# Kernel optimization log

Measured on AMD Instinct MI355X. Metric: run time of the kernel, lower is better.

The kernel has to match this reference:

```python
import jax, jax.numpy as jnp
import numpy as np

N_QUBITS = 16
DIM = 1 << N_QUBITS
NUM_CLASSES = 23
BATCH = 64

# PauliZ sign table: wire 0 is the most-significant bit of the flattened index.
_idx = np.arange(DIM)
SIGNS = np.stack([1 - 2 * ((_idx >> (N_QUBITS - 1 - w)) & 1) for w in range(N_QUBITS)], axis=1).astype(np.float32)  # (DIM, 16)


def _rx_mat(theta):
    c = jnp.cos(theta / 2).astype(jnp.complex64)
    s = (-1j * jnp.sin(theta / 2)).astype(jnp.complex64)
    return jnp.stack([jnp.stack([c, s]), jnp.stack([s, c])])  # (2,2)


def _rot_mat(phi, theta, omega):
    ct = jnp.cos(theta / 2)
    st = jnp.sin(theta / 2)
    a = jnp.exp(-0.5j * (phi + omega)) * ct
    b = -jnp.exp(0.5j * (phi - omega)) * st
    c = jnp.exp(-0.5j * (phi - omega)) * st
    d = jnp.exp(0.5j * (phi + omega)) * ct
    return jnp.stack([jnp.stack([a, b]), jnp.stack([c, d])]).astype(jnp.complex64)


def _apply_1q(state, U, w):
    # state: (B, 2,...,2); shared 2x2 gate on wire w (axis w+1)
    st = jnp.tensordot(state, U, axes=[[w + 1], [1]])  # contracted axis moves to last
    return jnp.moveaxis(st, -1, w + 1)


def _apply_rx_batched(state, theta_b, w):
    # per-sample RX angles theta_b: (B,)
    half = theta_b / 2
    c = jnp.cos(half).astype(jnp.complex64)
    s = (-1j * jnp.sin(half)).astype(jnp.complex64)
    U = jnp.stack([jnp.stack([c, s], -1), jnp.stack([s, c], -1)], -2)  # (B,2,2)
    st = jnp.moveaxis(state, w + 1, -1)
    st = jnp.einsum('bji,b...i->b...j', U, st)
    return jnp.moveaxis(st, -1, w + 1)


def _apply_crx(state, theta, ctrl, tgt):
    s0 = jax.lax.index_in_dim(state, 0, axis=ctrl + 1, keepdims=False)
    s1 = jax.lax.index_in_dim(state, 1, axis=ctrl + 1, keepdims=False)
    tax = tgt + 1 if tgt < ctrl else tgt  # target axis after control axis removal
    U = _rx_mat(theta)
    s1 = jnp.moveaxis(jnp.tensordot(s1, U, axes=[[tax], [1]]), -1, tax)
    return jnp.stack([s0, s1], axis=ctrl + 1)


def _circuit(x, w0, x0, w1, x1):
    B = x.shape[0]
    state = jnp.zeros((B,) + (2,) * N_QUBITS, jnp.complex64)
    state = state.at[(slice(None),) + (0,) * N_QUBITS].set(1.0)
    for w, xc in ((w0, x0), (w1, x1)):
        for q in range(N_QUBITS):
            state = _apply_rx_batched(state, x[:, q], q)
        for q in range(N_QUBITS):
            state = _apply_1q(state, _rot_mat(w[q, 0], w[q, 1], w[q, 2]), q)
        for q in range(N_QUBITS):
            state = _apply_crx(state, xc[q], q, (q + 1) % N_QUBITS)
    probs = (state.real ** 2 + state.imag ** 2).reshape(B, DIM)
    return probs @ jnp.asarray(SIGNS)  # (B, 16) PauliZ expvals


def setup_inputs() -> dict:
    key = jax.random.key(0)
    ks = jax.random.split(key, 7)
    return {
        'x': jax.random.normal(ks[0], (BATCH, N_QUBITS), jnp.float32),
        'w0': jax.random.normal(ks[1], (N_QUBITS, 3), jnp.float32),
        'x0': jax.random.normal(ks[2], (N_QUBITS,), jnp.float32),
        'w1': jax.random.normal(ks[3], (N_QUBITS, 3), jnp.float32),
        'x1': jax.random.normal(ks[4], (N_QUBITS,), jnp.float32),
        'fc_w': jax.random.normal(ks[5], (NUM_CLASSES, N_QUBITS), jnp.float32) * 0.25,
        'fc_b': jax.random.normal(ks[6], (NUM_CLASSES,), jnp.float32) * 0.05,
    }


def reference(x, w0, x0, w1, x1, fc_w, fc_b):
    feats = _circuit(x, w0, x0, w1, x1)           # (B, 16)
    logits = feats @ fc_w.T + fc_b                # (B, 23)
    return jax.nn.log_softmax(logits, axis=1)
```

## Files before the change

kernel.cpp:

```cpp
#include <hip/hip_runtime.h>
#include <hip/hip_bf16.h>


#define DIM 65536
#define BATCH 64
#define PSTR 580


template<int RB>
__device__ __forceinline__ void g1q_reg(float* sr, float* si, const float* U) {
  float u00r=U[0],u00i=U[1],u01r=U[2],u01i=U[3],u10r=U[4],u10i=U[5],u11r=U[6],u11i=U[7];
#pragma unroll
  for (int k = 0; k < 8; ++k) {
    int lo = k & ((1<<RB)-1);
    int j0 = ((k >> RB) << (RB+1)) | lo;
    int j1 = j0 | (1<<RB);
    float a0r=sr[j0], a0i=si[j0], a1r=sr[j1], a1i=si[j1];
    sr[j0] = u00r*a0r - u00i*a0i + u01r*a1r - u01i*a1i;
    si[j0] = u00r*a0i + u00i*a0r + u01r*a1i + u01i*a1r;
    sr[j1] = u10r*a0r - u10i*a0i + u11r*a1r - u11i*a1i;
    si[j1] = u10r*a0i + u10i*a0r + u11r*a1i + u11i*a1r;
  }
}

template<int RB, int CB>
__device__ __forceinline__ void gsel_reg_cc(float* sr, float* si, const float* M0, const float* M1) {
  float a0=M0[0],a1=M0[1],a2=M0[2],a3=M0[3],a4=M0[4],a5=M0[5],a6=M0[6],a7=M0[7];
  float b0=M1[0],b1=M1[1],b2=M1[2],b3=M1[3],b4=M1[4],b5=M1[5],b6=M1[6],b7=M1[7];
#pragma unroll
  for (int k = 0; k < 8; ++k) {
    int lo = k & ((1<<RB)-1);
    int j0 = ((k >> RB) << (RB+1)) | lo;
    int j1 = j0 | (1<<RB);
    const bool c = ((j0 >> CB) & 1) != 0;
    float u00r=c?b0:a0, u00i=c?b1:a1, u01r=c?b2:a2, u01i=c?b3:a3;
    float u10r=c?b4:a4, u10i=c?b5:a5, u11r=c?b6:a6, u11i=c?b7:a7;
    float p0r=sr[j0], p0i=si[j0], p1r=sr[j1], p1i=si[j1];
    sr[j0] = u00r*p0r - u00i*p0i + u01r*p1r - u01i*p1i;
    si[j0] = u00r*p0i + u00i*p0r + u01r*p1i + u01i*p1r;
    sr[j1] = u10r*p0r - u10i*p0i + u11r*p1r - u11i*p1i;
    si[j1] = u10r*p0i + u10i*p0r + u11r*p1i + u11i*p1r;
  }
}

template<int RB>
__device__ __forceinline__ void gsel_reg_pred(float* sr, float* si, const float* M0,
                                              const float* M1, bool ctrl) {
  float u[8];
#pragma unroll
  for (int e = 0; e < 8; ++e) u[e] = ctrl ? M1[e] : M0[e];
  g1q_reg<RB>(sr, si, u);
}

template<int CB, int LB>
__device__ __forceinline__ void crx_reg_lane(float* sr, float* si, float c, float s) {
#pragma unroll
  for (int k = 0; k < 8; ++k) {
    int lo2 = k & ((1<<CB)-1);
    int j = ((((k >> CB) << (CB+1)) | lo2)) | (1<<CB);
    float pr = __shfl_xor(sr[j], 1<<LB, 64);
    float pi = __shfl_xor(si[j], 1<<LB, 64);
    float mr = sr[j], mi = si[j];
    sr[j] = c*mr + s*pi;
    si[j] = c*mi - s*pr;
  }
}

__device__ __forceinline__ int swz(int o) { return o ^ ((o>>4)&15) ^ ((o>>8)&15); }

__device__ __forceinline__ unsigned bfp(float r, float i) {
  unsigned ur = __float_as_uint(r), ui = __float_as_uint(i);
  ur = (ur + 0x7fffu + ((ur >> 16) & 1u)) >> 16;
  ui = (ui + 0x7fffu + ((ui >> 16) & 1u)) & 0xffff0000u;
  return (ur & 0xffffu) | ui;
}
__device__ __forceinline__ float bfr(unsigned u) { return __uint_as_float(u << 16); }
__device__ __forceinline__ float bfi(unsigned u) { return __uint_as_float(u & 0xffff0000u); }

#define MP(Pb, l, q, s) ((Pb) + (((l)*16+(q))*2+(s))*8)


__global__ __launch_bounds__(256) void pA(float2* __restrict__ pre2, float* __restrict__ P,
                                          const float* __restrict__ x, const float* __restrict__ w0,
                                          const float* __restrict__ x0, const float* __restrict__ w1,
                                          const float* __restrict__ x1, float* __restrict__ feats,
                                          int* __restrict__ ctr) {
  __shared__ float2 lds2[4096];
  int b = blockIdx.x;
  int t = threadIdx.x, lane = t & 63, wv = t >> 6;
  float* Pb = P + (size_t)b * PSTR;

  {
    float (*su)[8] = reinterpret_cast<float(*)[8]>(lds2);
    if (t < 16) feats[b*16 + t] = 0.f;
    if (t == 16) ctr[b] = 0;
    if (t < 32) {
      int l = t >> 4, q = t & 15;
      const float* W = (l ? w1 : w0) + q*3;
      float xa = 0.5f * x[b*16 + q];
      float cr = cosf(xa), sx = sinf(xa);
      float phi = W[0], th = W[1], om = W[2];
      float ct = cosf(0.5f*th), stt = sinf(0.5f*th);
      float po = 0.5f*(phi+om), pm = 0.5f*(phi-om);
      float ar =  cosf(po)*ct,  ai = -sinf(po)*ct;
      float br = -cosf(pm)*stt, bi = -sinf(pm)*stt;
      float cr2 = cosf(pm)*stt, ci2 = -sinf(pm)*stt;
      float dr =  cosf(po)*ct,  di =  sinf(po)*ct;
      float U[8];
      U[0] = ar*cr + bi*sx;   U[1] = ai*cr - br*sx;
      U[2] = ai*sx + br*cr;   U[3] = -ar*sx + bi*cr;
      U[4] = cr2*cr + di*sx;  U[5] = ci2*cr - dr*sx;
      U[6] = ci2*sx + dr*cr;  U[7] = -cr2*sx + di*cr;
      float* M0 = MP(Pb, l, q, 0);
      float* M1 = M0 + 8;
#pragma unroll
      for (int e = 0; e < 8; ++e) { M0[e] = U[e]; su[t][e] = U[e]; }
      if (q == 0) {
        float ang = l ? 0.5f*x0[15] : 0.f;
        float cg = cosf(ang), sg = sinf(ang);
        M1[0] =  cg*U[0] + sg*U[3];  M1[1] = cg*U[1] - sg*U[2];
        M1[2] =  sg*U[1] + cg*U[2];  M1[3] = -sg*U[0] + cg*U[3];
        M1[4] =  cg*U[4] + sg*U[7];  M1[5] = cg*U[5] - sg*U[6];
        M1[6] =  sg*U[5] + cg*U[6];  M1[7] = -sg*U[4] + cg*U[7];
      } else {
        float ang = 0.5f*(l ? x1[q-1] : x0[q-1]);
        float cg = cosf(ang), sg = sinf(ang);
        M1[0] = cg*U[0] + sg*U[5];  M1[1] = cg*U[1] - sg*U[4];
        M1[2] = cg*U[2] + sg*U[7];  M1[3] = cg*U[3] - sg*U[6];
        M1[4] = cg*U[4] + sg*U[1];  M1[5] = cg*U[5] - sg*U[0];
        M1[6] = cg*U[6] + sg*U[3];  M1[7] = cg*U[7] - sg*U[2];
      }
      if (t == 0) { Pb[576] = cosf(0.5f*x1[15]); Pb[577] = sinf(0.5f*x1[15]); }
    }
    __syncthreads();
    if (t == 0) {
      float T0r[8], T0i[8], T1r[8], T1i[8];
#pragma unroll
      for (int k = 0; k < 8; ++k) {
        int b2 = (k>>2)&1, b1 = (k>>1)&1, b0k = k&1;
        float xr = su[13][b2*4], xi = su[13][b2*4+1];
        float yr = su[14][b1*4], yi = su[14][b1*4+1];
        float zr = su[15][b0k*4], zi = su[15][b0k*4+1];
        float pr = xr*yr - xi*yi, pi = xr*yi + xi*yr;
        T0r[k] = pr*zr - pi*zi; T0i[k] = pr*zi + pi*zr;
      }
      float a12 = 0.5f*x0[12], c12 = cosf(a12), s12 = sinf(a12);
#pragma unroll
      for (int k = 0; k < 8; ++k) { T1r[k] = c12*T0r[k] + s12*T0i[k^4]; T1i[k] = c12*T0i[k] - s12*T0r[k^4]; }
      float a13 = 0.5f*x0[13], c13 = cosf(a13), s13 = sinf(a13);
      float n0r[8], n0i[8], n1r[8], n1i[8];
#pragma unroll
      for (int k = 0; k < 8; ++k) {
        if (k & 4) {
          n0r[k] = c13*T0r[k] + s13*T0i[k^2]; n0i[k] = c13*T0i[k] - s13*T0r[k^2];
          n1r[k] = c13*T1r[k] + s13*T1i[k^2]; n1i[k] = c13*T1i[k] - s13*T1r[k^2];
        } else { n0r[k]=T0r[k]; n0i[k]=T0i[k]; n1r[k]=T1r[k]; n1i[k]=T1i[k]; }
      }
      float a14 = 0.5f*x0[14], c14 = cosf(a14), s14 = sinf(a14);
      float Fr[2][8], Fi[2][8];
#pragma unroll
      for (int k = 0; k < 8; ++k) {
        float r0, i0, r1, i1;
        if (k & 2) {
          r0 = c14*n0r[k] + s14*n0i[k^1]; i0 = c14*n0i[k] - s14*n0r[k^1];
          r1 = c14*n1r[k] + s14*n1i[k^1]; i1 = c14*n1i[k] - s14*n1r[k^1];
        } else { r0=n0r[k]; i0=n0i[k]; r1=n1r[k]; i1=n1i[k]; }
        Fr[0][k] = r0; Fi[0][k] = i0; Fr[1][k] = r1; Fi[1][k] = i1;
      }
      const float* A = MP(Pb,0,12,0);
      const float* B = MP(Pb,0,12,1);
      float wr[2][2], wi[2][2];
      wr[0][0] = A[0]; wi[0][0] = A[1];  wr[1][0] = A[4]; wi[1][0] = A[5];
      wr[0][1] = B[0]; wi[0][1] = B[1];  wr[1][1] = B[4]; wi[1][1] = B[5];
      float* T2 = Pb + 512;
#pragma unroll
      for (int j0 = 0; j0 < 2; ++j0)
#pragma unroll
        for (int j1 = 0; j1 < 2; ++j1)
#pragma unroll
          for (int k = 0; k < 8; ++k) {
            float tr = Fr[j0][k], ti = Fi[j0][k];
            float fr = wr[j0][j1], fi = wi[j0][j1];
            T2[((j0*2 + j1)*8 + k)*2 + 0] = tr*fr - ti*fi;
            T2[((j0*2 + j1)*8 + k)*2 + 1] = tr*fi + ti*fr;
          }
    }
  }

  float sr[16], si[16];
#pragma unroll
  for (int r = 0; r < 16; ++r) { sr[r] = 0.f; si[r] = 0.f; }
  if (t == 0) sr[0] = 1.f;

  g1q_reg<3>(sr, si, MP(Pb,0,0,0));
  gsel_reg_cc<2,3>(sr, si, MP(Pb,0,1,0), MP(Pb,0,1,1));
  gsel_reg_cc<1,2>(sr, si, MP(Pb,0,2,0), MP(Pb,0,2,1));
  gsel_reg_cc<0,1>(sr, si, MP(Pb,0,3,0), MP(Pb,0,3,1));
  __syncthreads();
#pragma unroll
  for (int r = 0; r < 16; ++r) {
    int o = wv | (lane << 2) | (r << 8);
    lds2[swz(o) & 4095] = make_float2(sr[r], si[r]);
  }
  __syncthreads();
#pragma unroll
  for (int r = 0; r < 16; ++r) {
    int o = wv | (((lane>>4)&3) << 2) | (r << 4) | ((lane&15) << 8);
    float2 v = lds2[swz(o) & 4095]; sr[r] = v.x; si[r] = v.y;
  }
  gsel_reg_pred<3>(sr, si, MP(Pb,0,4,0), MP(Pb,0,4,1), (lane&1)!=0);
  gsel_reg_cc<2,3>(sr, si, MP(Pb,0,5,0), MP(Pb,0,5,1));
  gsel_reg_cc<1,2>(sr, si, MP(Pb,0,6,0), MP(Pb,0,6,1));
  gsel_reg_cc<0,1>(sr, si, MP(Pb,0,7,0), MP(Pb,0,7,1));
  __syncthreads();
#pragma unroll
  for (int r = 0; r < 16; ++r) {
    int o = wv | (((lane>>4)&3) << 2) | (r << 4) | ((lane&15) << 8);
    lds2[swz(o) & 4095] = make_float2(sr[r], si[r]);
  }
  __syncthreads();
#pragma unroll
  for (int r = 0; r < 16; ++r) {
    int o = r | (lane << 4) | (wv << 10);
    float2 v = lds2[swz(o) & 4095]; sr[r] = v.x; si[r] = v.y;
  }
  gsel_reg_pred<3>(sr, si, MP(Pb,0,8,0), MP(Pb,0,8,1), (lane&1)!=0);
  gsel_reg_cc<2,3>(sr, si, MP(Pb,0,9,0), MP(Pb,0,9,1));
  gsel_reg_cc<1,2>(sr, si, MP(Pb,0,10,0), MP(Pb,0,10,1));
  gsel_reg_cc<0,1>(sr, si, MP(Pb,0,11,0), MP(Pb,0,11,1));
#pragma unroll
  for (int r = 0; r < 16; ++r) {
    int paddr = ((lane>>4)&3) | (wv << 2) | (r << 4) | ((lane&15) << 8);
    pre2[(size_t)b*4096 + paddr] = make_float2(sr[r], si[r]);
  }
}


__global__ __launch_bounds__(512) void pB(unsigned* __restrict__ st, const float2* __restrict__ pre2,
                                          const float* __restrict__ P) {
  __shared__ float2 lds2[8192];
  int blk = blockIdx.x;
  int b = blk >> 3, m = blk & 7;
  int t = threadIdx.x, lane = t & 63, wv = t >> 6;
  const float* Pb = P + (size_t)b*PSTR;

  float sr[16], si[16];
  {
    const float4* src = (const float4*)(pre2 + (size_t)b*4096) + ((lane << 3) | ((wv&3) << 9));
#pragma unroll
    for (int g = 0; g < 8; ++g) {
      float4 v = src[g];
      sr[2*g] = v.x; si[2*g] = v.y; sr[2*g+1] = v.z; si[2*g+1] = v.w;
    }
    int k = ((wv>>2)&1) | ((m&3) << 1);
    const float* tf = Pb + 512 + ((((m>>2)&1)*2 + (lane&1))*8 + k)*2;
    float fr = tf[0], fi = tf[1];
    const float* M = ((wv>>2)&1) ? MP(Pb,1,0,1) : MP(Pb,1,0,0);
    float v8[8];
#pragma unroll
    for (int e = 0; e < 4; ++e) {
      v8[2*e]   = fr*M[2*e]   - fi*M[2*e+1];
      v8[2*e+1] = fr*M[2*e+1] + fi*M[2*e];
    }
    g1q_reg<3>(sr, si, v8);
  }
  gsel_reg_cc<2,3>(sr, si, MP(Pb,1,1,0), MP(Pb,1,1,1));
  gsel_reg_cc<1,2>(sr, si, MP(Pb,1,2,0), MP(Pb,1,2,1));
  gsel_reg_cc<0,1>(sr, si, MP(Pb,1,3,0), MP(Pb,1,3,1));
#pragma unroll
  for (int r = 0; r < 16; ++r) {
    int o = (lane&63) | ((wv&3) << 6) | (r << 8) | (((wv>>2)&1) << 12);
    lds2[swz(o) & 8191] = make_float2(sr[r], si[r]);
  }
  __syncthreads();
#pragma unroll
  for (int r = 0; r < 16; ++r) {
    int o = (lane&15) | (r << 4) | (((lane>>4)&3) << 8) | ((wv&3) << 10) | (((wv>>2)&1) << 12);
    float2 v = lds2[swz(o) & 8191]; sr[r] = v.x; si[r] = v.y;
  }
  gsel_reg_pred<3>(sr, si, MP(Pb,1,4,0), MP(Pb,1,4,1), (lane&16)!=0);
  gsel_reg_cc<2,3>(sr, si, MP(Pb,1,5,0), MP(Pb,1,5,1));
  gsel_reg_cc<1,2>(sr, si, MP(Pb,1,6,0), MP(Pb,1,6,1));
  gsel_reg_cc<0,1>(sr, si, MP(Pb,1,7,0), MP(Pb,1,7,1));
  __syncthreads();
#pragma unroll
  for (int r = 0; r < 16; ++r) {
    int o = (lane&15) | (r << 4) | (((lane>>4)&3) << 8) | ((wv&3) << 10) | (((wv>>2)&1) << 12);
    lds2[swz(o) & 8191] = make_float2(sr[r], si[r]);
  }
  __syncthreads();
#pragma unroll
  for (int r = 0; r < 16; ++r) {
    int o = r | ((lane&63) << 4) | ((wv&3) << 10) | (((wv>>2)&1) << 12);
    float2 v = lds2[swz(o) & 8191]; sr[r] = v.x; si[r] = v.y;
  }
  gsel_reg_pred<3>(sr, si, MP(Pb,1,8,0), MP(Pb,1,8,1), (lane&1)!=0);
  gsel_reg_cc<2,3>(sr, si, MP(Pb,1,9,0), MP(Pb,1,9,1));
  gsel_reg_cc<1,2>(sr, si, MP(Pb,1,10,0), MP(Pb,1,10,1));
  gsel_reg_cc<0,1>(sr, si, MP(Pb,1,11,0), MP(Pb,1,11,1));
  {
    int sbase = ((lane&63) << 4) | ((wv&3) << 10) | (((wv>>2)&1) << 12) | (m << 13);
    uint4* dst = (uint4*)(st + (size_t)b*DIM + sbase);
#pragma unroll
    for (int g = 0; g < 4; ++g)
      dst[g] = make_uint4(bfp(sr[4*g],si[4*g]), bfp(sr[4*g+1],si[4*g+1]),
                          bfp(sr[4*g+2],si[4*g+2]), bfp(sr[4*g+3],si[4*g+3]));
  }
}


__global__ __launch_bounds__(512) void p3(const unsigned* __restrict__ st, const float* __restrict__ P,
                                          float* __restrict__ feats, int* __restrict__ ctr,
                                          const float* __restrict__ fcw, const float* __restrict__ fcb,
                                          float* __restrict__ out) {
  int blk = blockIdx.x;
  int b = blk >> 3, n = blk & 7;
  int t = threadIdx.x, lane = t & 63, wv = t >> 6;
  const float* Pb = P + (size_t)b*PSTR;
  int base = (lane&31) | (wv << 5) | (n << 8) | ((lane>>5) << 11);
  const unsigned* S = st + (size_t)b*DIM + base;
  float sr[16], si[16];
#pragma unroll
  for (int r = 0; r < 16; ++r) { unsigned u = S[r << 12]; sr[r] = bfr(u); si[r] = bfi(u); }

  gsel_reg_pred<3>(sr, si, MP(Pb,1,12,0), MP(Pb,1,12,1), (lane&1)!=0);
  gsel_reg_cc<2,3>(sr, si, MP(Pb,1,13,0), MP(Pb,1,13,1));
  gsel_reg_cc<1,2>(sr, si, MP(Pb,1,14,0), MP(Pb,1,14,1));
  gsel_reg_cc<0,1>(sr, si, MP(Pb,1,15,0), MP(Pb,1,15,1));
  crx_reg_lane<0,5>(sr, si, Pb[576], Pb[577]);

  float tot=0.f, sA=0.f, sB=0.f, sC=0.f, sD=0.f;
#pragma unroll
  for (int r = 0; r < 16; ++r) {
    float p = sr[r]*sr[r] + si[r]*si[r];
    tot += p;
    sA += (r & 1) ? -p : p;
    sB += (r & 2) ? -p : p;
    sC += (r & 4) ? -p : p;
    sD += (r & 8) ? -p : p;
  }
  float f[16];
  f[15] = sA; f[14] = sB; f[13] = sC; f[12] = sD;
  f[11] = (lane&1)  ? -tot : tot;
  f[10] = (lane&2)  ? -tot : tot;
  f[9]  = (lane&4)  ? -tot : tot;
  f[8]  = (lane&8)  ? -tot : tot;
  f[7]  = (lane&16) ? -tot : tot;
  f[0]  = (lane&32) ? -tot : tot;
  f[6]  = (wv&1)    ? -tot : tot;
  f[5]  = (wv&2)    ? -tot : tot;
  f[4]  = (wv&4)    ? -tot : tot;
  f[3]  = (n&1)     ? -tot : tot;
  f[2]  = (n&2)     ? -tot : tot;
  f[1]  = (n&4)     ? -tot : tot;
#pragma unroll
  for (int w = 0; w < 16; ++w) {
#pragma unroll
    for (int off = 32; off; off >>= 1) f[w] += __shfl_xor(f[w], off, 64);
  }
  __shared__ float red[8][17];
  if (lane == 0) {
#pragma unroll
    for (int w = 0; w < 16; ++w) red[wv][w] = f[w];
  }
  __syncthreads();
  if (t < 16) {
    float acc = 0.f;
#pragma unroll
    for (int i = 0; i < 8; ++i) acc += red[i][t];
    atomicAdd(&feats[b*16 + t], acc);
  }

  __shared__ int flagS;
  __syncthreads();
  if (t == 0) { __threadfence(); flagS = atomicAdd(&ctr[b], 1); }
  __syncthreads();
  if (flagS == 7) {
    __shared__ float fs[16];
    __shared__ float lg[23];
    if (t < 16) fs[t] = __hip_atomic_load(&feats[b*16 + t], __ATOMIC_RELAXED, __HIP_MEMORY_SCOPE_AGENT);
    __syncthreads();
    if (t < 23) {
      float acc = fcb[t];
#pragma unroll
      for (int w = 0; w < 16; ++w) acc += fs[w] * fcw[t*16 + w];
      lg[t] = acc;
    }
    __syncthreads();
    if (t < 23) {
      float mx = -1e30f;
#pragma unroll
      for (int j = 0; j < 23; ++j) mx = fmaxf(mx, lg[j]);
      float Ssum = 0.f;
#pragma unroll
      for (int j = 0; j < 23; ++j) Ssum += expf(lg[j] - mx);
      out[b*23 + t] = lg[t] - mx - logf(Ssum);
    }
  }
}

extern "C" void kernel_launch(void* const* d_in, const int* in_sizes, int n_in,
                              void* d_out, int out_size, void* d_ws, size_t ws_size,
                              hipStream_t stream) {
  const float* x   = (const float*)d_in[0];
  const float* w0  = (const float*)d_in[1];
  const float* x0  = (const float*)d_in[2];
  const float* w1  = (const float*)d_in[3];
  const float* x1  = (const float*)d_in[4];
  const float* fcw = (const float*)d_in[5];
  const float* fcb = (const float*)d_in[6];
  float* out = (float*)d_out;

  char* ws = (char*)d_ws;
  unsigned* st  = (unsigned*)ws;
  float2* pre2  = (float2*)(ws + (size_t)BATCH * DIM * 4);
  float*  P     = (float*)((char*)pre2 + (size_t)BATCH * 4096 * 8);
  float*  feats = P + (size_t)BATCH * PSTR;
  int*    ctr   = (int*)(feats + BATCH*16);

  pA<<<BATCH, 256, 0, stream>>>(pre2, P, x, w0, x0, w1, x1, feats, ctr);
  pB<<<512, 512, 0, stream>>>(st, pre2, P);
  p3<<<512, 512, 0, stream>>>(st, P, feats, ctr, fcw, fcb, out);
  (void)in_sizes; (void)n_in; (void)out_size; (void)ws_size;
}
```

Before: 125.3 us.

## Fuse first-layer precompute kernel into second-stage kernel with redundant per-block recompute

Removes the separate pA launch by having each of the 8 blocks per sample recompute the gate matrices and the 4096-amplitude first-layer prefix state in shared memory, instead of writing it to global memory (pre2) and reading it back. The serial single-thread T2 table construction is also parallelised across 8 lanes using warp shuffles. This saves one kernel launch and a global round-trip, but each sample's prefix work is now done 8 times and half the threads of each block sit idle during that phase.

Result: no change. 126.4 us (+0.9%).

```diff
diff --git a/kernel.cpp b/kernel.cpp
--- a/kernel.cpp
+++ b/kernel.cpp
@@ -80,20 +80,21 @@
 #define MP(Pb, l, q, s) ((Pb) + (((l)*16+(q))*2+(s))*8)
 
 
-__global__ __launch_bounds__(256) void pA(float2* __restrict__ pre2, float* __restrict__ P,
+__global__ __launch_bounds__(512) void pB(unsigned* __restrict__ st,
                                           const float* __restrict__ x, const float* __restrict__ w0,
                                           const float* __restrict__ x0, const float* __restrict__ w1,
-                                          const float* __restrict__ x1, float* __restrict__ feats,
-                                          int* __restrict__ ctr) {
-  __shared__ float2 lds2[4096];
-  int b = blockIdx.x;
+                                          const float* __restrict__ x1, float* __restrict__ P,
+                                          float* __restrict__ feats, int* __restrict__ ctr) {
+  __shared__ float2 lds2[8192];
+  __shared__ float Ps[PSTR];
+  int blk = blockIdx.x;
+  int b = blk >> 3, m = blk & 7;
   int t = threadIdx.x, lane = t & 63, wv = t >> 6;
-  float* Pb = P + (size_t)b * PSTR;
 
   {
     float (*su)[8] = reinterpret_cast<float(*)[8]>(lds2);
-    if (t < 16) feats[b*16 + t] = 0.f;
-    if (t == 16) ctr[b] = 0;
+    if (m == 0 && t < 16) feats[b*16 + t] = 0.f;
+    if (m == 0 && t == 16) ctr[b] = 0;
     if (t < 32) {
       int l = t >> 4, q = t & 15;
       const float* W = (l ? w1 : w0) + q*3;
@@ -111,7 +112,7 @@
       U[2] = ai*sx + br*cr;   U[3] = -ar*sx + bi*cr;
       U[4] = cr2*cr + di*sx;  U[5] = ci2*cr - dr*sx;
       U[6] = ci2*sx + dr*cr;  U[7] = -cr2*sx + di*cr;
-      float* M0 = MP(Pb, l, q, 0);
+      float* M0 = MP(Ps, l, q, 0);
       float* M1 = M0 + 8;
 #pragma unroll
       for (int e = 0; e < 8; ++e) { M0[e] = U[e]; su[t][e] = U[e]; }
@@ -130,132 +131,123 @@
         M1[4] = cg*U[4] + sg*U[1];  M1[5] = cg*U[5] - sg*U[0];
         M1[6] = cg*U[6] + sg*U[3];  M1[7] = cg*U[7] - sg*U[2];
       }
-      if (t == 0) { Pb[576] = cosf(0.5f*x1[15]); Pb[577] = sinf(0.5f*x1[15]); }
+      if (t == 0) { Ps[576] = cosf(0.5f*x1[15]); Ps[577] = sinf(0.5f*x1[15]); }
     }
     __syncthreads();
-    if (t == 0) {
-      float T0r[8], T0i[8], T1r[8], T1i[8];
-#pragma unroll
-      for (int k = 0; k < 8; ++k) {
-        int b2 = (k>>2)&1, b1 = (k>>1)&1, b0k = k&1;
-        float xr = su[13][b2*4], xi = su[13][b2*4+1];
-        float yr = su[14][b1*4], yi = su[14][b1*4+1];
-        float zr = su[15][b0k*4], zi = su[15][b0k*4+1];
-        float pr = xr*yr - xi*yi, pi = xr*yi + xi*yr;
-        T0r[k] = pr*zr - pi*zi; T0i[k] = pr*zi + pi*zr;
+  }
+
+  float sr[16], si[16];
+  if (t < 256) {
+#pragma unroll
+    for (int r = 0; r < 16; ++r) { sr[r] = 0.f; si[r] = 0.f; }
+    if (t == 0) sr[0] = 1.f;
+    g1q_reg<3>(sr, si, MP(Ps,0,0,0));
+    gsel_reg_cc<2,3>(sr, si, MP(Ps,0,1,0), MP(Ps,0,1,1));
+    gsel_reg_cc<1,2>(sr, si, MP(Ps,0,2,0), MP(Ps,0,2,1));
+    gsel_reg_cc<0,1>(sr, si, MP(Ps,0,3,0), MP(Ps,0,3,1));
+  } else if (t < 264) {
+    float (*su)[8] = reinterpret_cast<float(*)[8]>(lds2);
+    int k = t - 256;
+    float xr = su[13][((k>>2)&1)*4], xi = su[13][((k>>2)&1)*4+1];
+    float yr = su[14][((k>>1)&1)*4], yi = su[14][((k>>1)&1)*4+1];
+    float zr = su[15][(k&1)*4],      zi = su[15][(k&1)*4+1];
+    float pr = xr*yr - xi*yi, pi = xr*yi + xi*yr;
+    float T0r = pr*zr - pi*zi, T0i = pr*zi + pi*zr;
+    float a12 = 0.5f*x0[12], c12 = cosf(a12), s12 = sinf(a12);
+    float T0r4 = __shfl_xor(T0r, 4, 64), T0i4 = __shfl_xor(T0i, 4, 64);
+    float T1r = c12*T0r + s12*T0i4, T1i = c12*T0i - s12*T0r4;
+    float a13 = 0.5f*x0[13], c13 = cosf(a13), s13 = sinf(a13);
+    float T0r2 = __shfl_xor(T0r, 2, 64), T0i2 = __shfl_xor(T0i, 2, 64);
+    float T1r2 = __shfl_xor(T1r, 2, 64), T1i2 = __shfl_xor(T1i, 2, 64);
+    float n0r, n0i, n1r, n1i;
+    if (k & 4) {
+      n0r = c13*T0r + s13*T0i2; n0i = c13*T0i - s13*T0r2;
+      n1r = c13*T1r + s13*T1i2; n1i = c13*T1i - s13*T1r2;
+    } else { n0r = T0r; n0i = T0i; n1r = T1r; n1i = T1i; }
+    float a14 = 0.5f*x0[14], c14 = cosf(a14), s14 = sinf(a14);
+    float n0r1 = __shfl_xor(n0r, 1, 64), n0i1 = __shfl_xor(n0i, 1, 64);
+    float n1r1 = __shfl_xor(n1r, 1, 64), n1i1 = __shfl_xor(n1i, 1, 64);
+    float F0r, F0i, F1r, F1i;
+    if (k & 2) {
+      F0r = c14*n0r + s14*n0i1; F0i = c14*n0i - s14*n0r1;
+      F1r = c14*n1r + s14*n1i1; F1i = c14*n1i - s14*n1r1;
+    } else { F0r = n0r; F0i = n0i; F1r = n1r; F1i = n1i; }
+    const float* A = MP(Ps,0,12,0);
+    const float* B = MP(Ps,0,12,1);
+    float* T2 = Ps + 512;
+#pragma unroll
+    for (int j0 = 0; j0 < 2; ++j0) {
+      float tr = j0 ? F1r : F0r, ti = j0 ? F1i : F0i;
+#pragma unroll
+      for (int j1 = 0; j1 < 2; ++j1) {
+        const float* Wm = j1 ? B : A;
+        float fr = Wm[j0*4], fi = Wm[j0*4+1];
+        T2[((j0*2 + j1)*8 + k)*2 + 0] = tr*fr - ti*fi;
+        T2[((j0*2 + j1)*8 + k)*2 + 1] = tr*fi + ti*fr;
       }
-      float a12 = 0.5f*x0[12], c12 = cosf(a12), s12 = sinf(a12);
-#pragma unroll
-      for (int k = 0; k < 8; ++k) { T1r[k] = c12*T0r[k] + s12*T0i[k^4]; T1i[k] = c12*T0i[k] - s12*T0r[k^4]; }
-      float a13 = 0.5f*x0[13], c13 = cosf(a13), s13 = sinf(a13);
-      float n0r[8], n0i[8], n1r[8], n1i[8];
-#pragma unroll
-      for (int k = 0; k < 8; ++k) {
-        if (k & 4) {
-          n0r[k] = c13*T0r[k] + s13*T0i[k^2]; n0i[k] = c13*T0i[k] - s13*T0r[k^2];
-          n1r[k] = c13*T1r[k] + s13*T1i[k^2]; n1i[k] = c13*T1i[k] - s13*T1r[k^2];
-        } else { n0r[k]=T0r[k]; n0i[k]=T0i[k]; n1r[k]=T1r[k]; n1i[k]=T1i[k]; }
-      }
-      float a14 = 0.5f*x0[14], c14 = cosf(a14), s14 = sinf(a14);
-      float Fr[2][8], Fi[2][8];
-#pragma unroll
-      for (int k = 0; k < 8; ++k) {
-        float r0, i0, r1, i1;
-        if (k & 2) {
-          r0 = c14*n0r[k] + s14*n0i[k^1]; i0 = c14*n0i[k] - s14*n0r[k^1];
-          r1 = c14*n1r[k] + s14*n1i[k^1]; i1 = c14*n1i[k] - s14*n1r[k^1];
-        } else { r0=n0r[k]; i0=n0i[k]; r1=n1r[k]; i1=n1i[k]; }
-        Fr[0][k] = r0; Fi[0][k] = i0; Fr[1][k] = r1; Fi[1][k] = i1;
-      }
-      const float* A = MP(Pb,0,12,0);
-      const float* B = MP(Pb,0,12,1);
-      float wr[2][2], wi[2][2];
-      wr[0][0] = A[0]; wi[0][0] = A[1];  wr[1][0] = A[4]; wi[1][0] = A[5];
-      wr[0][1] = B[0]; wi[0][1] = B[1];  wr[1][1] = B[4]; wi[1][1] = B[5];
-      float* T2 = Pb + 512;
-#pragma unroll
-      for (int j0 = 0; j0 < 2; ++j0)
-#pragma unroll
-        for (int j1 = 0; j1 < 2; ++j1)
-#pragma unroll
-          for (int k = 0; k < 8; ++k) {
-            float tr = Fr[j0][k], ti = Fi[j0][k];
-            float fr = wr[j0][j1], fi = wi[j0][j1];
-            T2[((j0*2 + j1)*8 + k)*2 + 0] = tr*fr - ti*fi;
-            T2[((j0*2 + j1)*8 + k)*2 + 1] = tr*fi + ti*fr;
-          }
-    }
-  }
-
-  float sr[16], si[16];
-#pragma unroll
-  for (int r = 0; r < 16; ++r) { sr[r] = 0.f; si[r] = 0.f; }
-  if (t == 0) sr[0] = 1.f;
-
-  g1q_reg<3>(sr, si, MP(Pb,0,0,0));
-  gsel_reg_cc<2,3>(sr, si, MP(Pb,0,1,0), MP(Pb,0,1,1));
-  gsel_reg_cc<1,2>(sr, si, MP(Pb,0,2,0), MP(Pb,0,2,1));
-  gsel_reg_cc<0,1>(sr, si, MP(Pb,0,3,0), MP(Pb,0,3,1));
-  __syncthreads();
-#pragma unroll
-  for (int r = 0; r < 16; ++r) {
-    int o = wv | (lane << 2) | (r << 8);
-    lds2[swz(o) & 4095] = make_float2(sr[r], si[r]);
-  }
-  __syncthreads();
-#pragma unroll
-  for (int r = 0; r < 16; ++r) {
-    int o = wv | (((lane>>4)&3) << 2) | (r << 4) | ((lane&15) << 8);
-    float2 v = lds2[swz(o) & 4095]; sr[r] = v.x; si[r] = v.y;
-  }
-  gsel_reg_pred<3>(sr, si, MP(Pb,0,4,0), MP(Pb,0,4,1), (lane&1)!=0);
-  gsel_reg_cc<2,3>(sr, si, MP(Pb,0,5,0), MP(Pb,0,5,1));
-  gsel_reg_cc<1,2>(sr, si, MP(Pb,0,6,0), MP(Pb,0,6,1));
-  gsel_reg_cc<0,1>(sr, si, MP(Pb,0,7,0), MP(Pb,0,7,1));
-  __syncthreads();
-#pragma unroll
-  for (int r = 0; r < 16; ++r) {
-    int o = wv | (((lane>>4)&3) << 2) | (r << 4) | ((lane&15) << 8);
-    lds2[swz(o) & 4095] = make_float2(sr[r], si[r]);
-  }
-  __syncthreads();
-#pragma unroll
-  for (int r = 0; r < 16; ++r) {
-    int o = r | (lane << 4) | (wv << 10);
-    float2 v = lds2[swz(o) & 4095]; sr[r] = v.x; si[r] = v.y;
-  }
-  gsel_reg_pred<3>(sr, si, MP(Pb,0,8,0), MP(Pb,0,8,1), (lane&1)!=0);
-  gsel_reg_cc<2,3>(sr, si, MP(Pb,0,9,0), MP(Pb,0,9,1));
-  gsel_reg_cc<1,2>(sr, si, MP(Pb,0,10,0), MP(Pb,0,10,1));
-  gsel_reg_cc<0,1>(sr, si, MP(Pb,0,11,0), MP(Pb,0,11,1));
-#pragma unroll
-  for (int r = 0; r < 16; ++r) {
-    int paddr = ((lane>>4)&3) | (wv << 2) | (r << 4) | ((lane&15) << 8);
-    pre2[(size_t)b*4096 + paddr] = make_float2(sr[r], si[r]);
-  }
-}
-
-
-__global__ __launch_bounds__(512) void pB(unsigned* __restrict__ st, const float2* __restrict__ pre2,
-                                          const float* __restrict__ P) {
-  __shared__ float2 lds2[8192];
-  int blk = blockIdx.x;
-  int b = blk >> 3, m = blk & 7;
-  int t = threadIdx.x, lane = t & 63, wv = t >> 6;
-  const float* Pb = P + (size_t)b*PSTR;
-
-  float sr[16], si[16];
+    }
+  }
+  if (m == 0) {
+    if (t >= 448) P[(size_t)b*PSTR + t] = Ps[t];
+    else if (t == 320) { P[(size_t)b*PSTR + 576] = Ps[576]; P[(size_t)b*PSTR + 577] = Ps[577]; }
+  }
+  __syncthreads();
+  if (t < 256) {
+#pragma unroll
+    for (int r = 0; r < 16; ++r) {
+      int o = wv | (lane << 2) | (r << 8);
+      lds2[swz(o) & 4095] = make_float2(sr[r], si[r]);
+    }
+  }
+  __syncthreads();
+  if (t < 256) {
+#pragma unroll
+    for (int r = 0; r < 16; ++r) {
+      int o = wv | (((lane>>4)&3) << 2) | (r << 4) | ((lane&15) << 8);
+      float2 v = lds2[swz(o) & 4095]; sr[r] = v.x; si[r] = v.y;
+    }
+    gsel_reg_pred<3>(sr, si, MP(Ps,0,4,0), MP(Ps,0,4,1), (lane&1)!=0);
+    gsel_reg_cc<2,3>(sr, si, MP(Ps,0,5,0), MP(Ps,0,5,1));
+    gsel_reg_cc<1,2>(sr, si, MP(Ps,0,6,0), MP(Ps,0,6,1));
+    gsel_reg_cc<0,1>(sr, si, MP(Ps,0,7,0), MP(Ps,0,7,1));
+  }
+  __syncthreads();
+  if (t < 256) {
+#pragma unroll
+    for (int r = 0; r < 16; ++r) {
+      int o = wv | (((lane>>4)&3) << 2) | (r << 4) | ((lane&15) << 8);
+      lds2[swz(o) & 4095] = make_float2(sr[r], si[r]);
+    }
+  }
+  __syncthreads();
+  if (t < 256) {
+#pragma unroll
+    for (int r = 0; r < 16; ++r) {
+      int o = r | (lane << 4) | (wv << 10);
+      float2 v = lds2[swz(o) & 4095]; sr[r] = v.x; si[r] = v.y;
+    }
+    gsel_reg_pred<3>(sr, si, MP(Ps,0,8,0), MP(Ps,0,8,1), (lane&1)!=0);
+    gsel_reg_cc<2,3>(sr, si, MP(Ps,0,9,0), MP(Ps,0,9,1));
+    gsel_reg_cc<1,2>(sr, si, MP(Ps,0,10,0), MP(Ps,0,10,1));
+    gsel_reg_cc<0,1>(sr, si, MP(Ps,0,11,0), MP(Ps,0,11,1));
+#pragma unroll
+    for (int r = 0; r < 16; ++r) {
+      int paddr = ((lane>>4)&3) | (wv << 2) | (r << 4) | ((lane&15) << 8);
+      lds2[4096 + swz(paddr)] = make_float2(sr[r], si[r]);
+    }
+  }
+  __syncthreads();
+
   {
-    const float4* src = (const float4*)(pre2 + (size_t)b*4096) + ((lane << 3) | ((wv&3) << 9));
-#pragma unroll
-    for (int g = 0; g < 8; ++g) {
-      float4 v = src[g];
-      sr[2*g] = v.x; si[2*g] = v.y; sr[2*g+1] = v.z; si[2*g+1] = v.w;
+#pragma unroll
+    for (int r = 0; r < 16; ++r) {
+      int paddr = r | (lane << 4) | ((wv&3) << 10);
+      float2 v = lds2[4096 + swz(paddr)]; sr[r] = v.x; si[r] = v.y;
     }
     int k = ((wv>>2)&1) | ((m&3) << 1);
-    const float* tf = Pb + 512 + ((((m>>2)&1)*2 + (lane&1))*8 + k)*2;
+    const float* tf = Ps + 512 + ((((m>>2)&1)*2 + (lane&1))*8 + k)*2;
     float fr = tf[0], fi = tf[1];
-    const float* M = ((wv>>2)&1) ? MP(Pb,1,0,1) : MP(Pb,1,0,0);
+    const float* M = ((wv>>2)&1) ? MP(Ps,1,0,1) : MP(Ps,1,0,0);
     float v8[8];
 #pragma unroll
     for (int e = 0; e < 4; ++e) {
@@ -264,9 +256,10 @@
     }
     g1q_reg<3>(sr, si, v8);
   }
-  gsel_reg_cc<2,3>(sr, si, MP(Pb,1,1,0), MP(Pb,1,1,1));
-  gsel_reg_cc<1,2>(sr, si, MP(Pb,1,2,0), MP(Pb,1,2,1));
-  gsel_reg_cc<0,1>(sr, si, MP(Pb,1,3,0), MP(Pb,1,3,1));
+  gsel_reg_cc<2,3>(sr, si, MP(Ps,1,1,0), MP(Ps,1,1,1));
+  gsel_reg_cc<1,2>(sr, si, MP(Ps,1,2,0), MP(Ps,1,2,1));
+  gsel_reg_cc<0,1>(sr, si, MP(Ps,1,3,0), MP(Ps,1,3,1));
+  __syncthreads();
 #pragma unroll
   for (int r = 0; r < 16; ++r) {
     int o = (lane&63) | ((wv&3) << 6) | (r << 8) | (((wv>>2)&1) << 12);
@@ -278,10 +271,10 @@
     int o = (lane&15) | (r << 4) | (((lane>>4)&3) << 8) | ((wv&3) << 10) | (((wv>>2)&1) << 12);
     float2 v = lds2[swz(o) & 8191]; sr[r] = v.x; si[r] = v.y;
   }
-  gsel_reg_pred<3>(sr, si, MP(Pb,1,4,0), MP(Pb,1,4,1), (lane&16)!=0);
-  gsel_reg_cc<2,3>(sr, si, MP(Pb,1,5,0), MP(Pb,1,5,1));
-  gsel_reg_cc<1,2>(sr, si, MP(Pb,1,6,0), MP(Pb,1,6,1));
-  gsel_reg_cc<0,1>(sr, si, MP(Pb,1,7,0), MP(Pb,1,7,1));
+  gsel_reg_pred<3>(sr, si, MP(Ps,1,4,0), MP(Ps,1,4,1), (lane&16)!=0);
+  gsel_reg_cc<2,3>(sr, si, MP(Ps,1,5,0), MP(Ps,1,5,1));
+  gsel_reg_cc<1,2>(sr, si, MP(Ps,1,6,0), MP(Ps,1,6,1));
+  gsel_reg_cc<0,1>(sr, si, MP(Ps,1,7,0), MP(Ps,1,7,1));
   __syncthreads();
 #pragma unroll
   for (int r = 0; r < 16; ++r) {
@@ -294,10 +287,10 @@
     int o = r | ((lane&63) << 4) | ((wv&3) << 10) | (((wv>>2)&1) << 12);
     float2 v = lds2[swz(o) & 8191]; sr[r] = v.x; si[r] = v.y;
   }
-  gsel_reg_pred<3>(sr, si, MP(Pb,1,8,0), MP(Pb,1,8,1), (lane&1)!=0);
-  gsel_reg_cc<2,3>(sr, si, MP(Pb,1,9,0), MP(Pb,1,9,1));
-  gsel_reg_cc<1,2>(sr, si, MP(Pb,1,10,0), MP(Pb,1,10,1));
-  gsel_reg_cc<0,1>(sr, si, MP(Pb,1,11,0), MP(Pb,1,11,1));
+  gsel_reg_pred<3>(sr, si, MP(Ps,1,8,0), MP(Ps,1,8,1), (lane&1)!=0);
+  gsel_reg_cc<2,3>(sr, si, MP(Ps,1,9,0), MP(Ps,1,9,1));
+  gsel_reg_cc<1,2>(sr, si, MP(Ps,1,10,0), MP(Ps,1,10,1));
+  gsel_reg_cc<0,1>(sr, si, MP(Ps,1,11,0), MP(Ps,1,11,1));
   {
     int sbase = ((lane&63) << 4) | ((wv&3) << 10) | (((wv>>2)&1) << 12) | (m << 13);
     uint4* dst = (uint4*)(st + (size_t)b*DIM + sbase);
@@ -413,13 +406,11 @@
 
   char* ws = (char*)d_ws;
   unsigned* st  = (unsigned*)ws;
-  float2* pre2  = (float2*)(ws + (size_t)BATCH * DIM * 4);
-  float*  P     = (float*)((char*)pre2 + (size_t)BATCH * 4096 * 8);
+  float*  P     = (float*)(ws + (size_t)BATCH * DIM * 4);
   float*  feats = P + (size_t)BATCH * PSTR;
   int*    ctr   = (int*)(feats + BATCH*16);
 
-  pA<<<BATCH, 256, 0, stream>>>(pre2, P, x, w0, x0, w1, x1, feats, ctr);
-  pB<<<512, 512, 0, stream>>>(st, pre2, P);
+  pB<<<512, 512, 0, stream>>>(st, x, w0, x0, w1, x1, P, feats, ctr);
   p3<<<512, 512, 0, stream>>>(st, P, feats, ctr, fcw, fcb, out);
   (void)in_sizes; (void)n_in; (void)out_size; (void)ws_size;
 }
```
